# Kernel tuning notes

Hardware: AMD Instinct MI355X
Metric: run time of the kernel (lower is better)

Reference implementation:

```python
import jax, jax.numpy as jnp
import numpy as np

B = 32768
T = 30
H = 384


def setup_inputs() -> dict:
    key = jax.random.key(0)
    ks = jax.random.split(key, 16)

    def lin(k, out_d, in_d):
        # torch nn.Linear init: U(-1/sqrt(in_d), 1/sqrt(in_d))
        bound = 1.0 / np.sqrt(in_d)
        kw, kb = jax.random.split(k)
        W = jax.random.uniform(kw, (out_d, in_d), jnp.float32, -bound, bound)
        b = jax.random.uniform(kb, (out_d,), jnp.float32, -bound, bound)
        return W, b

    Wp, bp = lin(ks[0], 128, 3)        # plan_input
    Ws, bs = lin(ks[1], 128, 3)        # state_input
    # GRUCell params: weight_ih [3H,128], weight_hh [3H,H], init U(-1/sqrt(H),..)
    gb = 1.0 / np.sqrt(H)
    W_ih = jax.random.uniform(ks[2], (3 * H, 128), jnp.float32, -gb, gb)
    b_ih = jax.random.uniform(ks[3], (3 * H,), jnp.float32, -gb, gb)
    W_hh = jax.random.uniform(ks[4], (3 * H, H), jnp.float32, -gb, gb)
    b_hh = jax.random.uniform(ks[5], (3 * H,), jnp.float32, -gb, gb)
    Wd1, bd1 = lin(ks[6], 64, H)       # decode Linear(384,64)
    Wd2, bd2 = lin(ks[7], 3, 64)       # decode Linear(64,3)

    init_hidden = jax.random.normal(ks[8], (B, H), jnp.float32)
    plan = jax.random.normal(ks[9], (B, T, 3), jnp.float32)
    gate = jax.random.uniform(ks[10], (B, 1), jnp.float32)
    init_state = jax.random.normal(ks[11], (B, 3), jnp.float32)

    return {
        "init_hidden": init_hidden, "plan": plan, "gate": gate,
        "init_state": init_state,
        "Wp": Wp, "bp": bp, "Ws": Ws, "bs": bs,
        "W_ih": W_ih, "b_ih": b_ih, "W_hh": W_hh, "b_hh": b_hh,
        "Wd1": Wd1, "bd1": bd1, "Wd2": Wd2, "bd2": bd2,
    }


def reference(init_hidden, plan, gate, init_state,
              Wp, bp, Ws, bs, W_ih, b_ih, W_hh, b_hh,
              Wd1, bd1, Wd2, bd2):
    # Dropout(0.1) is identity in eval mode.
    plan_seq = jnp.swapaxes(plan[:, :T, :3], 0, 1)  # [T,B,3]

    def step(carry, plan_t):
        hidden, state = carry  # [B,H], [B,3]
        x = (state @ Ws.T + bs) + (plan_t @ Wp.T + bp) * gate  # [B,128]
        gi = x @ W_ih.T + b_ih          # [B,3H]
        gh = hidden @ W_hh.T + b_hh     # [B,3H]
        ir, iz, inn = jnp.split(gi, 3, axis=-1)
        hr, hz, hn = jnp.split(gh, 3, axis=-1)
        r = jax.nn.sigmoid(ir + hr)
        z = jax.nn.sigmoid(iz + hz)
        n = jnp.tanh(inn + r * hn)
        hidden = (1.0 - z) * n + z * hidden
        dec = jax.nn.elu(hidden @ Wd1.T + bd1) @ Wd2.T + bd2  # [B,3]
        state = dec + state
        return (hidden, state), state

    _, outs = jax.lax.scan(step, (init_hidden, init_state[:, :3]), plan_seq)
    return jnp.swapaxes(outs, 0, 1)  # [B,T,3]
```

## Files before the change

### kernel.cpp

```cpp
#include <hip/hip_runtime.h>


#define TT  30
#define NPH 50
#define PHU 12288
#define HS  392

typedef unsigned short u16;
typedef __bf16 bf16x8 __attribute__((ext_vector_type(8)));
typedef u16    u16x8  __attribute__((ext_vector_type(8)));
typedef float  f32x16 __attribute__((ext_vector_type(16)));

__device__ __forceinline__ u16 f2b(float f){
  unsigned u = __float_as_uint(f);
  u += 0x7FFFu + ((u >> 16) & 1u);
  return (u16)(u >> 16);
}
__device__ __forceinline__ float b2f(u16 h){ return __uint_as_float(((unsigned)h) << 16); }

__device__ __forceinline__ f32x16 mfma32(u16x8 a, u16x8 b, f32x16 c){
  return __builtin_amdgcn_mfma_f32_32x32x16_bf16(
      __builtin_bit_cast(bf16x8, a), __builtin_bit_cast(bf16x8, b), c, 0, 0, 0);
}
__device__ __forceinline__ void lds_fence(){ asm volatile("s_waitcnt lgkmcnt(0)" ::: "memory"); }
__device__ __forceinline__ void vm_fence(){ asm volatile("s_waitcnt vmcnt(0)" ::: "memory"); }
__device__ __forceinline__ float sigf(float x){ return __builtin_amdgcn_rcpf(1.f + __expf(-x)); }
__device__ __forceinline__ float tanh_(float x){ return 2.f*__builtin_amdgcn_rcpf(1.f + __expf(-2.f*x)) - 1.f; }

__device__ __forceinline__ void stage16(const u16* g, u16* l){
  __builtin_amdgcn_global_load_lds(
      (const __attribute__((address_space(1))) unsigned int*)g,
      (__attribute__((address_space(3))) unsigned int*)l, 16, 0, 0);
}

__global__ void prep_kernel(const float* __restrict__ Wih, const float* __restrict__ Whh,
                            const float* __restrict__ Wd1, const float* __restrict__ Wd2,
                            const float* __restrict__ bih, const float* __restrict__ bhh,
                            const float* __restrict__ Ws,  const float* __restrict__ bs,
                            const float* __restrict__ Wp,  const float* __restrict__ bp,
                            u16* __restrict__ stream, u16* __restrict__ wd2p,
                            u16* __restrict__ wxp, float* __restrict__ gb)
{
  int i = blockIdx.x*blockDim.x + threadIdx.x;
  if (i < 442368){
    int row = i/384, k = i - row*384;
    int g = row/384, unit = row - g*384, c = unit>>5, lc = unit&31;
    int kf = k>>4, hl = (k>>3)&1, j = k&7;
    int phase = c*4 + 1 + g;
    stream[(size_t)phase*PHU + kf*512 + (lc+32*hl)*8 + j] = f2b(Whh[i]);
  }
  if (i < 147456){
    int row = i>>7, k = i&127;
    int g = row/384, unit = row - g*384, c = unit>>5, lc = unit&31;
    int kf = k>>4, hl = (k>>3)&1, j = k&7;
    int phase = c*4;
    stream[(size_t)phase*PHU + (g*8+kf)*512 + (lc+32*hl)*8 + j] = f2b(Wih[i]);
  }
  if (i < 24576){
    int row = i/384, k = i - row*384;
    int ct = row>>5, lc = row&31;
    int kf = k>>4, hl = (k>>3)&1, j = k&7;
    int phase = 48 + ct;
    stream[(size_t)phase*PHU + kf*512 + (lc+32*hl)*8 + j] = f2b(Wd1[i]);
  }
  if (i < 2048){
    int kf = i>>9, r = i&511;
    int n = (r>>3)&31, hl = r>>8, j = r&7;
    int k = kf*16 + hl*8 + j;
    wd2p[i] = f2b((n<3) ? Wd2[n*64 + k] : 0.f);
  }
  if (i < 2048){
    int tl = i>>9, r = i&511;
    int n = (r>>3)&31, hl = r>>8, j = r&7;
    int k = hl*8 + j, u = tl*32 + n;
    float v = 0.f;
    if      (k <= 2) v = Ws[u*3 + k];
    else if (k == 3) v = bs[u];
    else if (k <= 6) v = Wp[u*3 + (k-4)];
    else if (k == 7) v = bp[u];
    wxp[i] = f2b(v);
  }
  if (i < 384){
    gb[i*4+0] = bih[i]       + bhh[i];
    gb[i*4+1] = bih[384+i]   + bhh[384+i];
    gb[i*4+2] = bih[768+i];
    gb[i*4+3] = bhh[768+i];
  }
}

__global__ __launch_bounds__(256, 1)
void gru_main(const float* __restrict__ ih, const float* __restrict__ plan,
              const float* __restrict__ gate, const float* __restrict__ istate,
              const u16* __restrict__ stream, const u16* __restrict__ wd2p,
              const u16* __restrict__ wxp, const float* __restrict__ gb,
              const float* __restrict__ bd1, const float* __restrict__ bd2,
              float* __restrict__ out)
{
  __shared__ __attribute__((aligned(16))) u16 wb[2][PHU];
  __shared__ __attribute__((aligned(16))) u16 hn[4][32*HS];
  __shared__ float sst[4][32][4];

  const int tid  = threadIdx.x;
  const int wave = tid >> 6, lane = tid & 63;
  const int m    = lane & 31, hl = lane >> 5;
  const int R0   = blockIdx.x*128 + wave*32;
  u16* hw = hn[wave];

  const float gt    = gate[R0 + m];
  const float bd1v0 = bd1[m], bd1v1 = bd1[32+m];
  const float bd2v  = (m<3) ? bd2[m] : 0.f;

  if (lane < 32){
    const float* sp = istate + (size_t)(R0+lane)*3;
    sst[wave][lane][0]=sp[0]; sst[wave][lane][1]=sp[1];
    sst[wave][lane][2]=sp[2]; sst[wave][lane][3]=0.f;
  }

  u16x8 hold[24];
#pragma unroll
  for (int kf=0; kf<24; ++kf){
    const float* p = ih + (size_t)(R0+m)*384 + kf*16 + hl*8;
    float4 a = *(const float4*)p;
    float4 b = *(const float4*)(p+4);
    u16x8 v;
    v[0]=f2b(a.x); v[1]=f2b(a.y); v[2]=f2b(a.z); v[3]=f2b(a.w);
    v[4]=f2b(b.x); v[5]=f2b(b.y); v[6]=f2b(b.z); v[7]=f2b(b.w);
    hold[kf]=v;
    *(u16x8*)&hw[m*HS + kf*16 + hl*8] = v;
  }

  const u16* srcb = stream + wave*3072 + lane*8;
  auto stage = [&](int ph, int bsel){
    const u16* s = srcb + (size_t)ph*PHU;
    u16* d = &wb[bsel][wave*3072];
#pragma unroll
    for (int ii=0; ii<6; ++ii) stage16(s + ii*512, d + ii*512);
  };

  stage(0, 0);
  vm_fence(); __syncthreads();
  int buf = 0, gp = 0;

#pragma unroll 1
  for (int t=0; t<TT; ++t){
    u16x8 a8;
    {
      float4 sv = *(const float4*)&sst[wave][m][0];
      const float* pp = plan + (size_t)(R0+m)*(TT*3) + t*3;
      float f0=sv.x, f1=sv.y, f2=sv.z, f3=1.f;
      float f4=gt*pp[0], f5=gt*pp[1], f6=gt*pp[2], f7=gt;
      if (hl){ a8[0]=0;a8[1]=0;a8[2]=0;a8[3]=0;a8[4]=0;a8[5]=0;a8[6]=0;a8[7]=0; }
      else { a8[0]=f2b(f0);a8[1]=f2b(f1);a8[2]=f2b(f2);a8[3]=f2b(f3);
             a8[4]=f2b(f4);a8[5]=f2b(f5);a8[6]=f2b(f6);a8[7]=f2b(f7); }
    }
    u16x8 xf[8];
#pragma unroll
    for (int tl=0; tl<4; ++tl){
      f32x16 ax;
#pragma unroll
      for (int r=0;r<16;++r) ax[r]=0.f;
      ax = mfma32(a8, *(const u16x8*)(wxp + tl*512 + lane*8), ax);
#pragma unroll
      for (int r=0;r<16;++r){
        int row = (r&3) + ((r>>2)<<3) + 4*hl;
        hw[row*HS + m] = f2b(ax[r]);
      }
      lds_fence();
      xf[2*tl]   = *(const u16x8*)&hw[m*HS + hl*8];
      xf[2*tl+1] = *(const u16x8*)&hw[m*HS + 16 + hl*8];
      lds_fence();
    }
    *(u16x8*)&hw[m*HS + hl*8]      = hold[0];
    *(u16x8*)&hw[m*HS + 16 + hl*8] = hold[1];
    lds_fence();

#pragma unroll 1
    for (int c=0; c<12; ++c){
      f32x16 aR, aZ, aNI, aNH;
      {
        const float4 b4 = *(const float4*)(gb + (size_t)(c*32+m)*4);
#pragma unroll
        for (int r=0;r<16;++r){ aR[r]=b4.x; aZ[r]=b4.y; aNI[r]=b4.z; aNH[r]=b4.w; }
      }
      {
        int np = gp+1; stage(np, buf^1);
        const u16* W = wb[buf];
#pragma unroll
        for (int kf=0; kf<8; ++kf){
          u16x8 bR = *(const u16x8*)(W + (kf    )*512 + lane*8);
          u16x8 bZ = *(const u16x8*)(W + (8+kf  )*512 + lane*8);
          u16x8 bN = *(const u16x8*)(W + (16+kf )*512 + lane*8);
          aR  = mfma32(xf[kf], bR, aR);
          aZ  = mfma32(xf[kf], bZ, aZ);
          aNI = mfma32(xf[kf], bN, aNI);
        }
        vm_fence(); __syncthreads(); buf^=1; gp=np;
      }
      {
        int np = gp+1; stage(np, buf^1);
        const u16* W = wb[buf];
#pragma unroll
        for (int kf=0; kf<24; ++kf)
          aR = mfma32(hold[kf], *(const u16x8*)(W + kf*512 + lane*8), aR);
        vm_fence(); __syncthreads(); buf^=1; gp=np;
      }
      {
        int np = gp+1; stage(np, buf^1);
        const u16* W = wb[buf];
#pragma unroll
        for (int kf=0; kf<24; ++kf)
          aZ = mfma32(hold[kf], *(const u16x8*)(W + kf*512 + lane*8), aZ);
        vm_fence(); __syncthreads(); buf^=1; gp=np;
      }
      {
        int np = gp+1; stage(np, buf^1);
        const u16* W = wb[buf];
#pragma unroll
        for (int kf=0; kf<24; ++kf)
          aNH = mfma32(hold[kf], *(const u16x8*)(W + kf*512 + lane*8), aNH);
#pragma unroll
        for (int r=0;r<16;++r){
          int row = (r&3) + ((r>>2)<<3) + 4*hl;
          float rr = sigf(aR[r]);
          float zz = sigf(aZ[r]);
          float nn = tanh_(aNI[r] + rr*aNH[r]);
          int off = row*HS + c*32 + m;
          float ho = b2f(hw[off]);
          hw[off] = f2b((1.f-zz)*nn + zz*ho);
        }
        vm_fence(); __syncthreads(); buf^=1; gp=np;
      }
    }

    lds_fence();
#pragma unroll
    for (int kf=0; kf<24; ++kf)
      hold[kf] = *(const u16x8*)&hw[m*HS + kf*16 + hl*8];

    f32x16 a0, a1;
#pragma unroll
    for (int r=0;r<16;++r){ a0[r]=bd1v0; a1[r]=bd1v1; }
    {
      int np = gp+1; stage(np, buf^1);
      const u16* W = wb[buf];
#pragma unroll
      for (int kf=0; kf<24; ++kf)
        a0 = mfma32(hold[kf], *(const u16x8*)(W + kf*512 + lane*8), a0);
      vm_fence(); __syncthreads(); buf^=1; gp=np;
    }
    {
      int np = (gp+1 == NPH) ? 0 : gp+1;
      stage(np, buf^1);
      const u16* W = wb[buf];
#pragma unroll
      for (int kf=0; kf<24; ++kf)
        a1 = mfma32(hold[kf], *(const u16x8*)(W + kf*512 + lane*8), a1);

      u16x8 wd2f0 = *(const u16x8*)(wd2p + 0*512 + lane*8);
      u16x8 wd2f1 = *(const u16x8*)(wd2p + 1*512 + lane*8);
      u16x8 wd2f2 = *(const u16x8*)(wd2p + 2*512 + lane*8);
      u16x8 wd2f3 = *(const u16x8*)(wd2p + 3*512 + lane*8);

      f32x16 ao;
#pragma unroll
      for (int r=0;r<16;++r) ao[r]=0.f;
#pragma unroll
      for (int r=0;r<16;++r){
        int row = (r&3) + ((r>>2)<<3) + 4*hl;
        float e = a0[r]; e = e>0.f ? e : (__expf(e)-1.f);
        hw[row*HS + m] = f2b(e);
      }
      lds_fence();
      {
        u16x8 af0 = *(const u16x8*)&hw[m*HS + hl*8];
        u16x8 af1 = *(const u16x8*)&hw[m*HS + 16 + hl*8];
        ao = mfma32(af0, wd2f0, ao);
        ao = mfma32(af1, wd2f1, ao);
      }
      lds_fence();
#pragma unroll
      for (int r=0;r<16;++r){
        int row = (r&3) + ((r>>2)<<3) + 4*hl;
        float e = a1[r]; e = e>0.f ? e : (__expf(e)-1.f);
        hw[row*HS + m] = f2b(e);
      }
      lds_fence();
      {
        u16x8 af0 = *(const u16x8*)&hw[m*HS + hl*8];
        u16x8 af1 = *(const u16x8*)&hw[m*HS + 16 + hl*8];
        ao = mfma32(af0, wd2f2, ao);
        ao = mfma32(af1, wd2f3, ao);
      }
      lds_fence();
      *(u16x8*)&hw[m*HS + hl*8]      = hold[0];
      *(u16x8*)&hw[m*HS + 16 + hl*8] = hold[1];

#pragma unroll
      for (int r=0;r<16;++r){
        int row = (r&3) + ((r>>2)<<3) + 4*hl;
        if (m < 3){
          float ns = sst[wave][row][m] + ao[r] + bd2v;
          out[(size_t)(R0+row)*(TT*3) + t*3 + m] = ns;
          sst[wave][row][m] = ns;
        }
      }
      vm_fence(); __syncthreads(); buf^=1; gp=np;
    }
  }
}

extern "C" void kernel_launch(void* const* d_in, const int* in_sizes, int n_in,
                              void* d_out, int out_size, void* d_ws, size_t ws_size,
                              hipStream_t stream)
{
  (void)in_sizes; (void)n_in; (void)out_size; (void)ws_size;
  const float* ih     = (const float*)d_in[0];
  const float* plan   = (const float*)d_in[1];
  const float* gatep  = (const float*)d_in[2];
  const float* istate = (const float*)d_in[3];
  const float* Wp     = (const float*)d_in[4];
  const float* bp     = (const float*)d_in[5];
  const float* Ws     = (const float*)d_in[6];
  const float* bs     = (const float*)d_in[7];
  const float* Wih    = (const float*)d_in[8];
  const float* bih    = (const float*)d_in[9];
  const float* Whh    = (const float*)d_in[10];
  const float* bhh    = (const float*)d_in[11];
  const float* Wd1    = (const float*)d_in[12];
  const float* bd1    = (const float*)d_in[13];
  const float* Wd2    = (const float*)d_in[14];
  const float* bd2    = (const float*)d_in[15];

  u16*   wstream = (u16*)d_ws;
  u16*   wd2p    = (u16*)((char*)d_ws + 1228800);
  u16*   wxp     = (u16*)((char*)d_ws + 1232896);
  float* gb      = (float*)((char*)d_ws + 1236992);

  prep_kernel<<<1728, 256, 0, stream>>>(Wih, Whh, Wd1, Wd2, bih, bhh, Ws, bs, Wp, bp,
                                        wstream, wd2p, wxp, gb);
  gru_main<<<256, 256, 0, stream>>>(ih, plan, gatep, istate,
                                    wstream, wd2p, wxp, gb, bd1, bd2, (float*)d_out);
}
```

Measured before the change: 1.729 ms.

## Load MFMA weight fragments directly from global instead of LDS double-buffer

Removes the double-buffered LDS weight staging (global_load_lds plus a block-wide barrier per phase). Each wave now reads its B-operand fragments straight from a re-laid-out global weight array, relying on L2/L1 caching since every block reads the same weights. This drops about fifty __syncthreads per timestep and frees 48KB of LDS. In exchange, MFMA operands now wait on global-memory latency with no explicit prefetch, and each of the four waves fetches the weights separately rather than sharing one staged copy.

```diff
diff --git a/kernel.cpp b/kernel.cpp
--- a/kernel.cpp
+++ b/kernel.cpp
@@ -2,8 +2,6 @@
 
 
 #define TT  30
-#define NPH 50
-#define PHU 12288
 #define HS  392
 
 typedef unsigned short u16;
@@ -23,45 +21,35 @@
       __builtin_bit_cast(bf16x8, a), __builtin_bit_cast(bf16x8, b), c, 0, 0, 0);
 }
 __device__ __forceinline__ void lds_fence(){ asm volatile("s_waitcnt lgkmcnt(0)" ::: "memory"); }
-__device__ __forceinline__ void vm_fence(){ asm volatile("s_waitcnt vmcnt(0)" ::: "memory"); }
 __device__ __forceinline__ float sigf(float x){ return __builtin_amdgcn_rcpf(1.f + __expf(-x)); }
 __device__ __forceinline__ float tanh_(float x){ return 2.f*__builtin_amdgcn_rcpf(1.f + __expf(-2.f*x)) - 1.f; }
-
-__device__ __forceinline__ void stage16(const u16* g, u16* l){
-  __builtin_amdgcn_global_load_lds(
-      (const __attribute__((address_space(1))) unsigned int*)g,
-      (__attribute__((address_space(3))) unsigned int*)l, 16, 0, 0);
-}
 
 __global__ void prep_kernel(const float* __restrict__ Wih, const float* __restrict__ Whh,
                             const float* __restrict__ Wd1, const float* __restrict__ Wd2,
                             const float* __restrict__ bih, const float* __restrict__ bhh,
                             const float* __restrict__ Ws,  const float* __restrict__ bs,
                             const float* __restrict__ Wp,  const float* __restrict__ bp,
-                            u16* __restrict__ stream, u16* __restrict__ wd2p,
+                            u16* __restrict__ sgl, u16* __restrict__ wd2p,
                             u16* __restrict__ wxp, float* __restrict__ gb)
 {
   int i = blockIdx.x*blockDim.x + threadIdx.x;
   if (i < 442368){
     int row = i/384, k = i - row*384;
-    int g = row/384, unit = row - g*384, c = unit>>5, lc = unit&31;
+    int g = row/384, u = row - g*384, c = u>>5, lc = u&31;
     int kf = k>>4, hl = (k>>3)&1, j = k&7;
-    int phase = c*4 + 1 + g;
-    stream[(size_t)phase*PHU + kf*512 + (lc+32*hl)*8 + j] = f2b(Whh[i]);
+    sgl[(size_t)(c*96 + 24 + g*24 + kf)*512 + (lc+32*hl)*8 + j] = f2b(Whh[i]);
   }
   if (i < 147456){
     int row = i>>7, k = i&127;
-    int g = row/384, unit = row - g*384, c = unit>>5, lc = unit&31;
+    int g = row/384, u = row - g*384, c = u>>5, lc = u&31;
     int kf = k>>4, hl = (k>>3)&1, j = k&7;
-    int phase = c*4;
-    stream[(size_t)phase*PHU + (g*8+kf)*512 + (lc+32*hl)*8 + j] = f2b(Wih[i]);
+    sgl[(size_t)(c*96 + g*8 + kf)*512 + (lc+32*hl)*8 + j] = f2b(Wih[i]);
   }
   if (i < 24576){
     int row = i/384, k = i - row*384;
-    int ct = row>>5, lc = row&31;
+    int nt = row>>5, lc = row&31;
     int kf = k>>4, hl = (k>>3)&1, j = k&7;
-    int phase = 48 + ct;
-    stream[(size_t)phase*PHU + kf*512 + (lc+32*hl)*8 + j] = f2b(Wd1[i]);
+    sgl[(size_t)(1152 + nt*24 + kf)*512 + (lc+32*hl)*8 + j] = f2b(Wd1[i]);
   }
   if (i < 2048){
     int kf = i>>9, r = i&511;
@@ -91,12 +79,11 @@
 __global__ __launch_bounds__(256, 1)
 void gru_main(const float* __restrict__ ih, const float* __restrict__ plan,
               const float* __restrict__ gate, const float* __restrict__ istate,
-              const u16* __restrict__ stream, const u16* __restrict__ wd2p,
+              const u16* __restrict__ sgl, const u16* __restrict__ wd2p,
               const u16* __restrict__ wxp, const float* __restrict__ gb,
               const float* __restrict__ bd1, const float* __restrict__ bd2,
               float* __restrict__ out)
 {
-  __shared__ __attribute__((aligned(16))) u16 wb[2][PHU];
   __shared__ __attribute__((aligned(16))) u16 hn[4][32*HS];
   __shared__ float sst[4][32][4];
 
@@ -128,18 +115,7 @@
     hold[kf]=v;
     *(u16x8*)&hw[m*HS + kf*16 + hl*8] = v;
   }
-
-  const u16* srcb = stream + wave*3072 + lane*8;
-  auto stage = [&](int ph, int bsel){
-    const u16* s = srcb + (size_t)ph*PHU;
-    u16* d = &wb[bsel][wave*3072];
-#pragma unroll
-    for (int ii=0; ii<6; ++ii) stage16(s + ii*512, d + ii*512);
-  };
-
-  stage(0, 0);
-  vm_fence(); __syncthreads();
-  int buf = 0, gp = 0;
+  lds_fence();
 
 #pragma unroll 1
   for (int t=0; t<TT; ++t){
@@ -176,59 +152,41 @@
 
 #pragma unroll 1
     for (int c=0; c<12; ++c){
+      const u16* gB = sgl + (size_t)c*96*512 + lane*8;
+
       f32x16 aR, aZ, aNI, aNH;
       {
         const float4 b4 = *(const float4*)(gb + (size_t)(c*32+m)*4);
 #pragma unroll
         for (int r=0;r<16;++r){ aR[r]=b4.x; aZ[r]=b4.y; aNI[r]=b4.z; aNH[r]=b4.w; }
       }
-      {
-        int np = gp+1; stage(np, buf^1);
-        const u16* W = wb[buf];
-#pragma unroll
-        for (int kf=0; kf<8; ++kf){
-          u16x8 bR = *(const u16x8*)(W + (kf    )*512 + lane*8);
-          u16x8 bZ = *(const u16x8*)(W + (8+kf  )*512 + lane*8);
-          u16x8 bN = *(const u16x8*)(W + (16+kf )*512 + lane*8);
-          aR  = mfma32(xf[kf], bR, aR);
-          aZ  = mfma32(xf[kf], bZ, aZ);
-          aNI = mfma32(xf[kf], bN, aNI);
-        }
-        vm_fence(); __syncthreads(); buf^=1; gp=np;
-      }
-      {
-        int np = gp+1; stage(np, buf^1);
-        const u16* W = wb[buf];
-#pragma unroll
-        for (int kf=0; kf<24; ++kf)
-          aR = mfma32(hold[kf], *(const u16x8*)(W + kf*512 + lane*8), aR);
-        vm_fence(); __syncthreads(); buf^=1; gp=np;
-      }
-      {
-        int np = gp+1; stage(np, buf^1);
-        const u16* W = wb[buf];
-#pragma unroll
-        for (int kf=0; kf<24; ++kf)
-          aZ = mfma32(hold[kf], *(const u16x8*)(W + kf*512 + lane*8), aZ);
-        vm_fence(); __syncthreads(); buf^=1; gp=np;
-      }
-      {
-        int np = gp+1; stage(np, buf^1);
-        const u16* W = wb[buf];
-#pragma unroll
-        for (int kf=0; kf<24; ++kf)
-          aNH = mfma32(hold[kf], *(const u16x8*)(W + kf*512 + lane*8), aNH);
-#pragma unroll
-        for (int r=0;r<16;++r){
-          int row = (r&3) + ((r>>2)<<3) + 4*hl;
-          float rr = sigf(aR[r]);
-          float zz = sigf(aZ[r]);
-          float nn = tanh_(aNI[r] + rr*aNH[r]);
-          int off = row*HS + c*32 + m;
-          float ho = b2f(hw[off]);
-          hw[off] = f2b((1.f-zz)*nn + zz*ho);
-        }
-        vm_fence(); __syncthreads(); buf^=1; gp=np;
+#pragma unroll
+      for (int kf=0; kf<8; ++kf){
+        u16x8 bR = *(const u16x8*)(gB + (     kf)*512);
+        u16x8 bZ = *(const u16x8*)(gB + ( 8 + kf)*512);
+        u16x8 bN = *(const u16x8*)(gB + (16 + kf)*512);
+        aR  = mfma32(xf[kf], bR, aR);
+        aZ  = mfma32(xf[kf], bZ, aZ);
+        aNI = mfma32(xf[kf], bN, aNI);
+      }
+#pragma unroll
+      for (int kf=0; kf<24; ++kf){
+        u16x8 bR = *(const u16x8*)(gB + (24 + kf)*512);
+        u16x8 bZ = *(const u16x8*)(gB + (48 + kf)*512);
+        u16x8 bN = *(const u16x8*)(gB + (72 + kf)*512);
+        aR  = mfma32(hold[kf], bR, aR);
+        aZ  = mfma32(hold[kf], bZ, aZ);
+        aNH = mfma32(hold[kf], bN, aNH);
+      }
+#pragma unroll
+      for (int r=0;r<16;++r){
+        int row = (r&3) + ((r>>2)<<3) + 4*hl;
+        float rr = sigf(aR[r]);
+        float zz = sigf(aZ[r]);
+        float nn = tanh_(aNI[r] + rr*aNH[r]);
+        int off = row*HS + c*32 + m;
+        float ho = b2f(hw[off]);
+        hw[off] = f2b((1.f-zz)*nn + zz*ho);
       }
     }
 
@@ -237,25 +195,18 @@
     for (int kf=0; kf<24; ++kf)
       hold[kf] = *(const u16x8*)&hw[m*HS + kf*16 + hl*8];
 
-    f32x16 a0, a1;
-#pragma unroll
-    for (int r=0;r<16;++r){ a0[r]=bd1v0; a1[r]=bd1v1; }
     {
-      int np = gp+1; stage(np, buf^1);
-      const u16* W = wb[buf];
-#pragma unroll
-      for (int kf=0; kf<24; ++kf)
-        a0 = mfma32(hold[kf], *(const u16x8*)(W + kf*512 + lane*8), a0);
-      vm_fence(); __syncthreads(); buf^=1; gp=np;
-    }
-    {
-      int np = (gp+1 == NPH) ? 0 : gp+1;
-      stage(np, buf^1);
-      const u16* W = wb[buf];
-#pragma unroll
-      for (int kf=0; kf<24; ++kf)
-        a1 = mfma32(hold[kf], *(const u16x8*)(W + kf*512 + lane*8), a1);
-
+      const u16* dB = sgl + (size_t)1152*512 + lane*8;
+      f32x16 a0, a1;
+#pragma unroll
+      for (int r=0;r<16;++r){ a0[r]=bd1v0; a1[r]=bd1v1; }
+#pragma unroll
+      for (int kf=0; kf<24; ++kf){
+        u16x8 b0 = *(const u16x8*)(dB + (     kf)*512);
+        a0 = mfma32(hold[kf], b0, a0);
+        u16x8 b1 = *(const u16x8*)(dB + (24 + kf)*512);
+        a1 = mfma32(hold[kf], b1, a1);
+      }
       u16x8 wd2f0 = *(const u16x8*)(wd2p + 0*512 + lane*8);
       u16x8 wd2f1 = *(const u16x8*)(wd2p + 1*512 + lane*8);
       u16x8 wd2f2 = *(const u16x8*)(wd2p + 2*512 + lane*8);
@@ -304,7 +255,7 @@
           sst[wave][row][m] = ns;
         }
       }
-      vm_fence(); __syncthreads(); buf^=1; gp=np;
+      lds_fence();
     }
   }
 }
@@ -331,13 +282,13 @@
   const float* Wd2    = (const float*)d_in[14];
   const float* bd2    = (const float*)d_in[15];
 
-  u16*   wstream = (u16*)d_ws;
-  u16*   wd2p    = (u16*)((char*)d_ws + 1228800);
-  u16*   wxp     = (u16*)((char*)d_ws + 1232896);
-  float* gb      = (float*)((char*)d_ws + 1236992);
+  u16*   sgl  = (u16*)d_ws;
+  u16*   wd2p = (u16*)((char*)d_ws + 1228800);
+  u16*   wxp  = (u16*)((char*)d_ws + 1232896);
+  float* gb   = (float*)((char*)d_ws + 1236992);
 
   prep_kernel<<<1728, 256, 0, stream>>>(Wih, Whh, Wd1, Wd2, bih, bhh, Ws, bs, Wp, bp,
-                                        wstream, wd2p, wxp, gb);
+                                        sgl, wd2p, wxp, gb);
   gru_main<<<256, 256, 0, stream>>>(ih, plan, gatep, istate,
-                                    wstream, wd2p, wxp, gb, bd1, bd2, (float*)d_out);
-}
+                                    sgl, wd2p, wxp, gb, bd1, bd2, (float*)d_out);
+}
```

Measured after the change: 2.239 ms. 1.29x slower.
